# Kernel optimization log

Measured on AMD Instinct MI355X. Metric: run time of the kernel, lower is better.

## Reference

```python
import jax, jax.numpy as jnp
import numpy as np

N_NODES = 50000
N_EDGES = 800000
NEG_SLOPE = 0.2  # PyG GATv2Conv default
EPS = 1e-16      # PyG softmax denominator epsilon


def _segment_softmax(logits, seg, num_segments):
    # logits: [E, H]; seg: [E] target-node ids
    m = jax.ops.segment_max(logits, seg, num_segments=num_segments)
    p = jnp.exp(logits - m[seg])
    s = jax.ops.segment_sum(p, seg, num_segments=num_segments)
    return p / (s[seg] + EPS)


def _gatv2_conv(x, src, dst, Wl, Wr, att, bias, heads, out_ch, concat):
    # x: [N, F]; Wl/Wr: [F, heads*out_ch]; att: [heads, out_ch]
    n = x.shape[0]
    xl = (x @ Wl).reshape(n, heads, out_ch)
    xr = (x @ Wr).reshape(n, heads, out_ch)
    # GATv2: e_ij = att . leaky_relu(xl[j] + xr[i]) for edge j->i
    e = jax.nn.leaky_relu(xl[src] + xr[dst], NEG_SLOPE)  # [E, H, C]
    logit = jnp.einsum('ehc,hc->eh', e, att)             # [E, H]
    alpha = _segment_softmax(logit, dst, n)              # [E, H]
    out = jax.ops.segment_sum(alpha[:, :, None] * xl[src], dst, num_segments=n)  # [N, H, C]
    if concat:
        out = out.reshape(n, heads * out_ch)
    else:
        out = out.mean(axis=1)
    return out + bias


def setup_inputs() -> dict:
    key = jax.random.key(0)
    ks = jax.random.split(key, 20)
    in_ch, hid, out_ch, heads, edge_dim = 128, 128, 64, 8, 6
    c1 = hid // heads  # 16
    g = lambda k, shp, fan: (jax.random.normal(k, shp, jnp.float32) / np.sqrt(fan)).astype(jnp.float32)
    inp = {
        'x': jax.random.normal(ks[0], (N_NODES, in_ch), jnp.float32),
        'edge_index': jax.random.randint(ks[1], (2, N_EDGES), 0, N_NODES, dtype=jnp.int64),
        'edge_attr': jax.random.normal(ks[2], (N_EDGES, edge_dim), jnp.float32),
        'Wl1': g(ks[3], (in_ch, heads * c1), in_ch),
        'Wr1': g(ks[4], (in_ch, heads * c1), in_ch),
        'att1': g(ks[5], (heads, c1), c1),
        'b1': jnp.zeros((heads * c1,), jnp.float32),
        # layer 2: GATv2Conv(hid -> out_ch, heads=1, no concat)
        'Wl2': g(ks[6], (hid, out_ch), hid),
        'Wr2': g(ks[7], (hid, out_ch), hid),
        'att2': g(ks[8], (1, out_ch), out_ch),
        'b2': jnp.zeros((out_ch,), jnp.float32),
        # edge encoder (computed but unused downstream, as in the source)
        'We1': g(ks[9], (edge_dim, hid), edge_dim), 'be1': jnp.zeros((hid,), jnp.float32),
        'We2': g(ks[10], (hid, hid), hid), 'be2': jnp.zeros((hid,), jnp.float32),
        # classifier
        'Wc1': g(ks[11], (out_ch, hid), out_ch), 'bc1': jnp.zeros((hid,), jnp.float32),
        'Wc2': g(ks[12], (hid, 2), hid), 'bc2': jnp.zeros((2,), jnp.float32),
    }
    return inp


def reference(x, edge_index, edge_attr, Wl1, Wr1, att1, b1, Wl2, Wr2, att2, b2,
              We1, be1, We2, be2, Wc1, bc1, Wc2, bc2):
    n = x.shape[0]
    # edge encoder (dead code in the original forward; kept for fidelity)
    _edge_feats = jax.nn.relu(edge_attr @ We1 + be1) @ We2 + be2
    # add self-loops (PyG GATv2Conv default add_self_loops=True)
    loop = jnp.arange(n, dtype=edge_index.dtype)
    src = jnp.concatenate([edge_index[0], loop])
    dst = jnp.concatenate([edge_index[1], loop])
    # layer 1 (heads=8, concat) + relu; dropout is identity in eval
    h = _gatv2_conv(x, src, dst, Wl1, Wr1, att1, b1, heads=8, out_ch=16, concat=True)
    h = jax.nn.relu(h)
    # layer 2 (heads=1, mean)
    emb = _gatv2_conv(h, src, dst, Wl2, Wr2, att2, b2, heads=1, out_ch=64, concat=False)
    logits = jax.nn.relu(emb @ Wc1 + bc1) @ Wc2 + bc2
    return emb, logits
```

## Files before the change

kernel.cpp:

```cpp
#include <hip/hip_runtime.h>
#include <hip/hip_bf16.h>
#include <cfloat>

#define N_NODES 50000
#define N_EDGES 800000
#define E_TOT   850000
#define NEG_SLOPE 0.2f
#define SM_EPS 1e-16f
#define SCAN_B 196

typedef __attribute__((ext_vector_type(8))) short short8;
typedef __attribute__((ext_vector_type(4))) float f32x4;

__device__ __forceinline__ float lrelu(float v) { return v > 0.0f ? v : NEG_SLOPE * v; }

__device__ __forceinline__ unsigned f2bf_pack2(float a, float b) {
    unsigned ua = __float_as_uint(a);
    ua += 0x7fff + ((ua >> 16) & 1);
    unsigned ub = __float_as_uint(b);
    ub += 0x7fff + ((ub >> 16) & 1);
    return (ua >> 16) | (ub & 0xffff0000u);
}
__device__ __forceinline__ unsigned short f2bf(float a) {
    unsigned ua = __float_as_uint(a);
    ua += 0x7fff + ((ua >> 16) & 1);
    return (unsigned short)(ua >> 16);
}
__device__ __forceinline__ float bf_lo(unsigned u) { return __uint_as_float(u << 16); }
__device__ __forceinline__ float bf_hi(unsigned u) { return __uint_as_float(u & 0xffff0000u); }

__device__ __forceinline__ unsigned short pack_one(const float* __restrict__ B0,
                                                   const float* __restrict__ B1,
                                                   int i, int N) {
    int m   = i / (128 * N);
    int rem = i % (128 * N);
    int j    = rem & 7;
    int quad = (rem >> 3) & 3;
    int n    = (rem >> 5) & 15;
    int ctk  = rem >> 9;
    int ct   = ctk % (N / 16);
    int kt   = ctk / (N / 16);
    int k    = kt * 32 + quad * 8 + j;
    int col  = ct * 16 + n;
    const float* B = m ? B1 : B0;
    return f2bf(B[k * N + col]);
}

__global__ void prep(const float* __restrict__ Wl1, const float* __restrict__ Wr1,
                     const float* __restrict__ Wl2, const float* __restrict__ Wr2,
                     unsigned short* __restrict__ Bp1, unsigned short* __restrict__ Bp2,
                     int* __restrict__ deg, int* __restrict__ flags) {
    int i = blockIdx.x * 256 + threadIdx.x;
    if (i < 32768) {
        Bp1[i] = pack_one(Wl1, Wr1, i, 128);
    } else if (i < 49152) {
        Bp2[i - 32768] = pack_one(Wl2, Wr2, i - 32768, 64);
    } else if (i < 99152) {
        deg[i - 49152] = 0;
    } else if (i < 99408) {
        flags[i - 99152] = 0;
    }
}

__device__ __forceinline__ void gemm128_half(int b, const float* __restrict__ x,
                                             const unsigned short* __restrict__ Bm,
                                             unsigned short* __restrict__ Cbf,
                                             float* __restrict__ Cf, int M) {
    int w = threadIdx.x >> 6, lane = threadIdx.x & 63;
    int quad = lane >> 4, l16 = lane & 15;
    int row0 = b * 32 + (w & 1) * 16;
    int cb   = (w >> 1) * 64;
    f32x4 acc[4];
    #pragma unroll
    for (int t = 0; t < 4; ++t) acc[t] = (f32x4){0.f, 0.f, 0.f, 0.f};
    int arow = row0 + l16;
    bool aok = arow < M;
    #pragma unroll
    for (int kt = 0; kt < 4; ++kt) {
        short8 a = (short8)0;
        if (aok) {
            const float* Ap = x + (size_t)arow * 128 + quad * 8 + kt * 32;
            float4 f0 = *(const float4*)(Ap);
            float4 f1 = *(const float4*)(Ap + 4);
            union { uint4 u; short8 s; } cv;
            cv.u.x = f2bf_pack2(f0.x, f0.y);
            cv.u.y = f2bf_pack2(f0.z, f0.w);
            cv.u.z = f2bf_pack2(f1.x, f1.y);
            cv.u.w = f2bf_pack2(f1.z, f1.w);
            a = cv.s;
        }
        #pragma unroll
        for (int t = 0; t < 4; ++t) {
            int ct = (cb >> 4) + t;
            const short* bp = (const short*)Bm + (((kt * 8 + ct) * 16 + l16) * 4 + quad) * 8;
            short8 bfr = *(const short8*)bp;
            acc[t] = __builtin_amdgcn_mfma_f32_16x16x32_bf16(a, bfr, acc[t], 0, 0, 0);
        }
    }
    #pragma unroll
    for (int t = 0; t < 4; ++t) {
        int col = cb + t * 16 + l16;
        #pragma unroll
        for (int r = 0; r < 4; ++r) {
            int row = row0 + quad * 4 + r;
            if (row < M) {
                if (Cbf) Cbf[(size_t)row * 128 + col] = f2bf(acc[t][r]);
                else     Cf[(size_t)row * 128 + col]  = acc[t][r];
            }
        }
    }
}

__global__ __launch_bounds__(256)
void k_count_gemmxl(const int* __restrict__ ei, int* __restrict__ deg,
                    unsigned short* __restrict__ rank16,
                    const float* __restrict__ x, const unsigned short* __restrict__ Bp1,
                    unsigned short* __restrict__ xlbf, int M) {
    int sub = blockIdx.x >> 1;
    if (blockIdx.x & 1) {
        int nz = __syncthreads_or(ei[2 * threadIdx.x + 1]);
        int i = sub * 256 + threadIdx.x;
        if (2 * i >= N_EDGES) return;
        bool has2 = (2 * i + 1 < N_EDGES);
        int d0, d1 = 0;
        if (nz) {
            int2 dp = *(const int2*)(ei + N_EDGES + 2 * i);
            d0 = dp.x; d1 = dp.y;
        } else {
            int4 dp = *(const int4*)(ei + 2 * N_EDGES + 4 * i);
            d0 = dp.x; d1 = dp.z;
        }
        unsigned short r0 = (unsigned short)atomicAdd(&deg[d0], 1);
        unsigned short r1 = 0;
        if (has2) r1 = (unsigned short)atomicAdd(&deg[d1], 1);
        *(unsigned int*)(rank16 + 2 * i) = (unsigned int)r0 | ((unsigned int)r1 << 16);
    } else {
        gemm128_half(sub, x, Bp1, xlbf, nullptr, M);
    }
}

__global__ void scan_fused(const int* __restrict__ deg, int* __restrict__ rowptr,
                           int* __restrict__ esrc, int* __restrict__ bsum,
                           int* __restrict__ flags) {
    __shared__ int sh[256];
    int b = blockIdx.x, t = threadIdx.x, i = b * 256 + t;
    int v = (i < N_NODES) ? deg[i] + 1 : 0;
    sh[t] = v;
    __syncthreads();
    int val = v;
    for (int off = 1; off < 256; off <<= 1) {
        int add = (t >= off) ? sh[t - off] : 0;
        __syncthreads();
        val += add; sh[t] = val;
        __syncthreads();
    }
    if (t == 255) {
        bsum[b] = val;
        __threadfence();
        atomicExch(&flags[b], 1);
    }
    int contrib = 0;
    if (t < b) {
        while (atomicAdd(&flags[t], 0) == 0) {}
        contrib = atomicAdd(&bsum[t], 0);
    }
    __syncthreads();
    sh[t] = contrib;
    __syncthreads();
    #pragma unroll
    for (int off = 128; off; off >>= 1) {
        if (t < off) sh[t] += sh[t + off];
        __syncthreads();
    }
    int offset = sh[0];
    if (i < N_NODES) {
        int rp = (val - v) + offset;
        rowptr[i] = rp;
        esrc[rp] = i;
    }
    if (i == 0) rowptr[N_NODES] = E_TOT;
}

__global__ __launch_bounds__(256)
void k_scatter_gemmxr(const int* __restrict__ ei, const int* __restrict__ rowptr,
                      const unsigned short* __restrict__ rank16, int* __restrict__ esrc,
                      const float* __restrict__ x, const unsigned short* __restrict__ Bp1,
                      float* __restrict__ xr1, int M) {
    int sub = blockIdx.x >> 1;
    if (blockIdx.x & 1) {
        int nz = __syncthreads_or(ei[2 * threadIdx.x + 1]);
        int i = sub * 256 + threadIdx.x;
        if (2 * i >= N_EDGES) return;
        bool has2 = (2 * i + 1 < N_EDGES);
        int s0, d0, s1 = 0, d1 = 0;
        if (nz) {
            int2 sp = *(const int2*)(ei + 2 * i);
            int2 dp = *(const int2*)(ei + N_EDGES + 2 * i);
            s0 = sp.x; s1 = sp.y; d0 = dp.x; d1 = dp.y;
        } else {
            int4 sp = *(const int4*)(ei + 4 * i);
            int4 dp = *(const int4*)(ei + 2 * N_EDGES + 4 * i);
            s0 = sp.x; s1 = sp.z; d0 = dp.x; d1 = dp.z;
        }
        unsigned int rr = *(const unsigned int*)(rank16 + 2 * i);
        esrc[rowptr[d0] + 1 + (int)(rr & 0xffffu)] = s0;
        if (has2) esrc[rowptr[d1] + 1 + (int)(rr >> 16)] = s1;
    } else {
        gemm128_half(sub, x, Bp1 + 128 * 128, nullptr, xr1, M);
    }
}

__global__ __launch_bounds__(256)
void gemm_mfma64(const unsigned short* __restrict__ Abf, const unsigned short* __restrict__ Bp,
                 unsigned short* __restrict__ C0bf, float* __restrict__ C1, int M) {
    int w = threadIdx.x >> 6, lane = threadIdx.x & 63;
    int quad = lane >> 4, l16 = lane & 15;
    int matrix = w >> 1;
    int row0 = blockIdx.x * 32 + (w & 1) * 16;
    const unsigned short* Bm = Bp + matrix * 128 * 64;
    f32x4 acc[4];
    #pragma unroll
    for (int t = 0; t < 4; ++t) acc[t] = (f32x4){0.f, 0.f, 0.f, 0.f};
    int arow = row0 + l16;
    bool aok = arow < M;
    const short* Ap = (const short*)Abf + (size_t)arow * 128 + quad * 8;
    #pragma unroll
    for (int kt = 0; kt < 4; ++kt) {
        short8 a = (short8)0;
        if (aok) a = *(const short8*)(Ap + kt * 32);
        #pragma unroll
        for (int t = 0; t < 4; ++t) {
            const short* bp = (const short*)Bm + (((kt * 4 + t) * 16 + l16) * 4 + quad) * 8;
            short8 bfr = *(const short8*)bp;
            acc[t] = __builtin_amdgcn_mfma_f32_16x16x32_bf16(a, bfr, acc[t], 0, 0, 0);
        }
    }
    #pragma unroll
    for (int t = 0; t < 4; ++t) {
        int col = t * 16 + l16;
        #pragma unroll
        for (int r = 0; r < 4; ++r) {
            int row = row0 + quad * 4 + r;
            if (row < M) {
                if (matrix) C1[(size_t)row * 64 + col] = acc[t][r];
                else        C0bf[(size_t)row * 64 + col] = f2bf(acc[t][r]);
            }
        }
    }
}

__global__ __launch_bounds__(256)
void node_fused1(const int* __restrict__ rowptr, const int* __restrict__ esrc,
                 const unsigned short* __restrict__ xlbf, const float* __restrict__ xr,
                 const float* __restrict__ att, const float* __restrict__ b1,
                 unsigned short* __restrict__ hbf) {
    int wave = threadIdx.x >> 6;
    int lane = threadIdx.x & 63;
    int n = blockIdx.x * 4 + wave;
    int slot = lane >> 4;
    int l = lane & 15;
    int beg = rowptr[n], end = rowptr[n + 1];
    const float* xrp = xr + (size_t)n * 128 + 8 * l;
    float4 xra = *(const float4*)(xrp);
    float4 xrb = *(const float4*)(xrp + 4);
    float4 ata = *(const float4*)(att + 8 * l);
    float4 atb = *(const float4*)(att + 8 * l + 4);
    float den = 0.0f;
    float4 aa = {0, 0, 0, 0}, ab = {0, 0, 0, 0};

    auto body = [&](int k) {
        int s = esrc[k];
        uint4 u = *(const uint4*)(xlbf + (size_t)s * 128 + 8 * l);
        float x0 = bf_lo(u.x), x1 = bf_hi(u.x);
        float x2 = bf_lo(u.y), x3 = bf_hi(u.y);
        float x4 = bf_lo(u.z), x5 = bf_hi(u.z);
        float x6 = bf_lo(u.w), x7 = bf_hi(u.w);
        float v = ata.x * lrelu(x0 + xra.x) + ata.y * lrelu(x1 + xra.y)
                + ata.z * lrelu(x2 + xra.z) + ata.w * lrelu(x3 + xra.w)
                + atb.x * lrelu(x4 + xrb.x) + atb.y * lrelu(x5 + xrb.y)
                + atb.z * lrelu(x6 + xrb.z) + atb.w * lrelu(x7 + xrb.w);
        v += __shfl_xor(v, 1);
        float p = __expf(v);
        den += p;
        aa.x += p * x0; aa.y += p * x1; aa.z += p * x2; aa.w += p * x3;
        ab.x += p * x4; ab.y += p * x5; ab.z += p * x6; ab.w += p * x7;
    };
    int k = beg + slot;
    for (; k + 4 < end; k += 8) { body(k); body(k + 4); }
    if (k < end) body(k);

    #pragma unroll
    for (int off = 16; off < 64; off <<= 1) {
        aa.x += __shfl_xor(aa.x, off); aa.y += __shfl_xor(aa.y, off);
        aa.z += __shfl_xor(aa.z, off); aa.w += __shfl_xor(aa.w, off);
        ab.x += __shfl_xor(ab.x, off); ab.y += __shfl_xor(ab.y, off);
        ab.z += __shfl_xor(ab.z, off); ab.w += __shfl_xor(ab.w, off);
        den   += __shfl_xor(den, off);
    }
    if (slot == 0) {
        float inv = 1.0f / (den + SM_EPS);
        float4 b4a = *(const float4*)(b1 + 8 * l);
        float4 b4b = *(const float4*)(b1 + 8 * l + 4);
        float oa0 = fmaxf(aa.x * inv + b4a.x, 0.0f);
        float oa1 = fmaxf(aa.y * inv + b4a.y, 0.0f);
        float oa2 = fmaxf(aa.z * inv + b4a.z, 0.0f);
        float oa3 = fmaxf(aa.w * inv + b4a.w, 0.0f);
        float ob0 = fmaxf(ab.x * inv + b4b.x, 0.0f);
        float ob1 = fmaxf(ab.y * inv + b4b.y, 0.0f);
        float ob2 = fmaxf(ab.z * inv + b4b.z, 0.0f);
        float ob3 = fmaxf(ab.w * inv + b4b.w, 0.0f);
        uint4 pk;
        pk.x = f2bf_pack2(oa0, oa1);
        pk.y = f2bf_pack2(oa2, oa3);
        pk.z = f2bf_pack2(ob0, ob1);
        pk.w = f2bf_pack2(ob2, ob3);
        *(uint4*)(hbf + (size_t)n * 128 + 8 * l) = pk;
    }
}

__global__ __launch_bounds__(256)
void node_fused2(const int* __restrict__ rowptr, const int* __restrict__ esrc,
                 const unsigned short* __restrict__ xlbf, const float* __restrict__ xr,
                 const float* __restrict__ att, const float* __restrict__ b2v,
                 float* __restrict__ out_emb) {
    int wave = threadIdx.x >> 6;
    int lane = threadIdx.x & 63;
    int n = blockIdx.x * 4 + wave;
    int slot = lane >> 3;
    int l = lane & 7;
    int beg = rowptr[n], end = rowptr[n + 1];
    const float* xrp = xr + (size_t)n * 64 + 8 * l;
    float4 xra = *(const float4*)(xrp);
    float4 xrb = *(const float4*)(xrp + 4);
    float4 ata = *(const float4*)(att + 8 * l);
    float4 atb = *(const float4*)(att + 8 * l + 4);
    float den = 0.0f;
    float4 aa = {0, 0, 0, 0}, ab = {0, 0, 0, 0};

    auto body = [&](int k) {
        int s = esrc[k];
        uint4 u = *(const uint4*)(xlbf + (size_t)s * 64 + 8 * l);
        float x0 = bf_lo(u.x), x1 = bf_hi(u.x);
        float x2 = bf_lo(u.y), x3 = bf_hi(u.y);
        float x4 = bf_lo(u.z), x5 = bf_hi(u.z);
        float x6 = bf_lo(u.w), x7 = bf_hi(u.w);
        float v = ata.x * lrelu(x0 + xra.x) + ata.y * lrelu(x1 + xra.y)
                + ata.z * lrelu(x2 + xra.z) + ata.w * lrelu(x3 + xra.w)
                + atb.x * lrelu(x4 + xrb.x) + atb.y * lrelu(x5 + xrb.y)
                + atb.z * lrelu(x6 + xrb.z) + atb.w * lrelu(x7 + xrb.w);
        v += __shfl_xor(v, 1);
        v += __shfl_xor(v, 2);
        v += __shfl_xor(v, 4);
        float p = __expf(v);
        den += p;
        aa.x += p * x0; aa.y += p * x1; aa.z += p * x2; aa.w += p * x3;
        ab.x += p * x4; ab.y += p * x5; ab.z += p * x6; ab.w += p * x7;
    };
    int k = beg + slot;
    for (; k + 8 < end; k += 16) { body(k); body(k + 8); }
    if (k < end) body(k);

    #pragma unroll
    for (int off = 8; off < 64; off <<= 1) {
        aa.x += __shfl_xor(aa.x, off); aa.y += __shfl_xor(aa.y, off);
        aa.z += __shfl_xor(aa.z, off); aa.w += __shfl_xor(aa.w, off);
        ab.x += __shfl_xor(ab.x, off); ab.y += __shfl_xor(ab.y, off);
        ab.z += __shfl_xor(ab.z, off); ab.w += __shfl_xor(ab.w, off);
        den   += __shfl_xor(den, off);
    }
    if (slot == 0) {
        float inv = 1.0f / (den + SM_EPS);
        float4 b4a = *(const float4*)(b2v + 8 * l);
        float4 b4b = *(const float4*)(b2v + 8 * l + 4);
        float4 ea, eb;
        ea.x = aa.x * inv + b4a.x; ea.y = aa.y * inv + b4a.y;
        ea.z = aa.z * inv + b4a.z; ea.w = aa.w * inv + b4a.w;
        eb.x = ab.x * inv + b4b.x; eb.y = ab.y * inv + b4b.y;
        eb.z = ab.z * inv + b4b.z; eb.w = ab.w * inv + b4b.w;
        float* op = out_emb + (size_t)n * 64 + 8 * l;
        *(float4*)(op)     = ea;
        *(float4*)(op + 4) = eb;
    }
}

#define CLS_NODES 32
__global__ __launch_bounds__(256)
void classifier(const float* __restrict__ emb, const float* __restrict__ Wc1,
                const float* __restrict__ bc1, const float* __restrict__ Wc2,
                const float* __restrict__ bc2, float* __restrict__ out_logits) {
    __shared__ float w1[64 * 128];
    __shared__ float eS[CLS_NODES][64];
    __shared__ float tS[CLS_NODES][132];
    int t = threadIdx.x;
    int n0 = blockIdx.x * CLS_NODES;
    for (int i = t; i < 64 * 128 / 4; i += 256)
        ((float4*)w1)[i] = ((const float4*)Wc1)[i];
    for (int i = t; i < CLS_NODES * 64 / 4; i += 256) {
        size_t off = (size_t)n0 * 64 + i * 4;
        float4 v = {0, 0, 0, 0};
        if (off + 3 < (size_t)N_NODES * 64) v = *(const float4*)(emb + off);
        ((float4*)eS)[i] = v;
    }
    __syncthreads();
    int jj = t & 127, half = t >> 7;
    for (int nn = half; nn < CLS_NODES; nn += 2) {
        float a0 = 0, a1 = 0, a2 = 0, a3 = 0;
        #pragma unroll
        for (int k = 0; k < 64; k += 4) {
            a0 += eS[nn][k]     * w1[(k)     * 128 + jj];
            a1 += eS[nn][k + 1] * w1[(k + 1) * 128 + jj];
            a2 += eS[nn][k + 2] * w1[(k + 2) * 128 + jj];
            a3 += eS[nn][k + 3] * w1[(k + 3) * 128 + jj];
        }
        tS[nn][jj] = fmaxf(bc1[jj] + (a0 + a1) + (a2 + a3), 0.0f);
    }
    __syncthreads();
    int node = t >> 3, seg = t & 7;
    float v0 = 0, v1 = 0;
    #pragma unroll
    for (int c = 0; c < 16; ++c) {
        float tv = tS[node][seg * 16 + c];
        v0 += tv * Wc2[2 * (seg * 16 + c)];
        v1 += tv * Wc2[2 * (seg * 16 + c) + 1];
    }
    v0 += __shfl_xor(v0, 1); v1 += __shfl_xor(v1, 1);
    v0 += __shfl_xor(v0, 2); v1 += __shfl_xor(v1, 2);
    v0 += __shfl_xor(v0, 4); v1 += __shfl_xor(v1, 4);
    int n = n0 + node;
    if (seg == 0 && n < N_NODES) {
        out_logits[(size_t)n * 2 + 0] = v0 + bc2[0];
        out_logits[(size_t)n * 2 + 1] = v1 + bc2[1];
    }
}

extern "C" void kernel_launch(void* const* d_in, const int* in_sizes, int n_in,
                              void* d_out, int out_size, void* d_ws, size_t ws_size,
                              hipStream_t stream) {
    const float* x    = (const float*)d_in[0];
    const int*   ei   = (const int*)d_in[1];
    const float* Wl1  = (const float*)d_in[3];
    const float* Wr1  = (const float*)d_in[4];
    const float* att1 = (const float*)d_in[5];
    const float* b1   = (const float*)d_in[6];
    const float* Wl2  = (const float*)d_in[7];
    const float* Wr2  = (const float*)d_in[8];
    const float* att2 = (const float*)d_in[9];
    const float* b2   = (const float*)d_in[10];
    const float* Wc1  = (const float*)d_in[15];
    const float* bc1  = (const float*)d_in[16];
    const float* Wc2  = (const float*)d_in[17];
    const float* bc2  = (const float*)d_in[18];

    float* ws = (float*)d_ws;
    int* deg    = (int*)ws;
    int* rowptr = deg + 50000;
    int* esrc   = rowptr + 50016;
    int* bsum   = esrc + 850000;
    int* flags  = bsum + 256;
    unsigned short* rank16 = (unsigned short*)(flags + 256);
    float* xr1          = ws + 1400448;
    unsigned short* xlbf = (unsigned short*)(ws + 7800448);
    unsigned short* hbf  = (unsigned short*)(ws + 11000448);
    unsigned short* Bp1  = (unsigned short*)(ws + 14200448);
    unsigned short* Bp2  = (unsigned short*)(ws + 14216832);

    float* out_emb    = (float*)d_out;
    float* out_logits = out_emb + (size_t)N_NODES * 64;

    prep<<<389, 256, 0, stream>>>(Wl1, Wr1, Wl2, Wr2, Bp1, Bp2, deg, flags);

    k_count_gemmxl<<<3126, 256, 0, stream>>>(ei, deg, rank16, x, Bp1, xlbf, N_NODES);

    scan_fused<<<SCAN_B, 256, 0, stream>>>(deg, rowptr, esrc, bsum, flags);

    k_scatter_gemmxr<<<3126, 256, 0, stream>>>(ei, rowptr, rank16, esrc, x, Bp1, xr1, N_NODES);

    node_fused1<<<12500, 256, 0, stream>>>(rowptr, esrc, xlbf, xr1, att1, b1, hbf);

    gemm_mfma64<<<1563, 256, 0, stream>>>(hbf, Bp2, xlbf, xr1, N_NODES);
    node_fused2<<<12500, 256, 0, stream>>>(rowptr, esrc, xlbf, xr1, att2, b2, out_emb);

    classifier<<<1563, 256, 0, stream>>>(out_emb, Wc1, bc1, Wc2, bc2, out_logits);
}
```

Measured before the change: 326.0 us.

## Move classifier to bf16 MFMA, regroup xr GEMM with count pass, use exp2

The classifier's first layer becomes a bf16 MFMA GEMM. It reads a new bf16 copy of the embedding written by node_fused2 and a Wc1 repacked in prep, and folds the ReLU and the second layer into shuffle reductions. The old version staged a 32KB fp32 Wc1 in LDS per block and ran scalar FMAs. The xr GEMM now runs in the degree-count kernel, so the scatter kernel is edge-only. The softmax exponentials use exp2f with att prescaled by log2e. The bf16 classifier input adds rounding error, and the emb output gains an extra write.

```diff
diff --git a/kernel.cpp b/kernel.cpp
--- a/kernel.cpp
+++ b/kernel.cpp
@@ -8,6 +8,7 @@
 #define NEG_SLOPE 0.2f
 #define SM_EPS 1e-16f
 #define SCAN_B 196
+#define LOG2E 1.4426950408889634f
 
 typedef __attribute__((ext_vector_type(8))) short short8;
 typedef __attribute__((ext_vector_type(4))) float f32x4;
@@ -48,17 +49,28 @@
 
 __global__ void prep(const float* __restrict__ Wl1, const float* __restrict__ Wr1,
                      const float* __restrict__ Wl2, const float* __restrict__ Wr2,
+                     const float* __restrict__ Wc1,
                      unsigned short* __restrict__ Bp1, unsigned short* __restrict__ Bp2,
+                     unsigned short* __restrict__ Wc1p,
                      int* __restrict__ deg, int* __restrict__ flags) {
     int i = blockIdx.x * 256 + threadIdx.x;
     if (i < 32768) {
         Bp1[i] = pack_one(Wl1, Wr1, i, 128);
     } else if (i < 49152) {
         Bp2[i - 32768] = pack_one(Wl2, Wr2, i - 32768, 64);
-    } else if (i < 99152) {
-        deg[i - 49152] = 0;
-    } else if (i < 99408) {
-        flags[i - 99152] = 0;
+    } else if (i < 57344) {
+        int idx = i - 49152;
+        int j    = idx & 7;
+        int quad = (idx >> 3) & 3;
+        int n    = (idx >> 5) & 15;
+        int ctk  = idx >> 9;
+        int ct   = ctk & 7;
+        int kt   = ctk >> 3;
+        Wc1p[idx] = f2bf(Wc1[(kt * 32 + quad * 8 + j) * 128 + ct * 16 + n]);
+    } else if (i < 107344) {
+        deg[i - 57344] = 0;
+    } else if (i < 107600) {
+        flags[i - 107344] = 0;
     }
 }
 
@@ -112,12 +124,13 @@
 }
 
 __global__ __launch_bounds__(256)
-void k_count_gemmxl(const int* __restrict__ ei, int* __restrict__ deg,
+void k2_count_gemms(const int* __restrict__ ei, int* __restrict__ deg,
                     unsigned short* __restrict__ rank16,
                     const float* __restrict__ x, const unsigned short* __restrict__ Bp1,
-                    unsigned short* __restrict__ xlbf, int M) {
-    int sub = blockIdx.x >> 1;
-    if (blockIdx.x & 1) {
+                    unsigned short* __restrict__ xlbf, float* __restrict__ xr1, int M) {
+    int kind = blockIdx.x % 3;
+    int sub  = blockIdx.x / 3;
+    if (kind == 1) {
         int nz = __syncthreads_or(ei[2 * threadIdx.x + 1]);
         int i = sub * 256 + threadIdx.x;
         if (2 * i >= N_EDGES) return;
@@ -134,8 +147,10 @@
         unsigned short r1 = 0;
         if (has2) r1 = (unsigned short)atomicAdd(&deg[d1], 1);
         *(unsigned int*)(rank16 + 2 * i) = (unsigned int)r0 | ((unsigned int)r1 << 16);
+    } else if (kind == 0) {
+        gemm128_half(sub, x, Bp1, xlbf, nullptr, M);
     } else {
-        gemm128_half(sub, x, Bp1, xlbf, nullptr, M);
+        gemm128_half(sub, x, Bp1 + 128 * 128, nullptr, xr1, M);
     }
 }
 
@@ -181,33 +196,26 @@
     if (i == 0) rowptr[N_NODES] = E_TOT;
 }
 
-__global__ __launch_bounds__(256)
-void k_scatter_gemmxr(const int* __restrict__ ei, const int* __restrict__ rowptr,
-                      const unsigned short* __restrict__ rank16, int* __restrict__ esrc,
-                      const float* __restrict__ x, const unsigned short* __restrict__ Bp1,
-                      float* __restrict__ xr1, int M) {
-    int sub = blockIdx.x >> 1;
-    if (blockIdx.x & 1) {
-        int nz = __syncthreads_or(ei[2 * threadIdx.x + 1]);
-        int i = sub * 256 + threadIdx.x;
-        if (2 * i >= N_EDGES) return;
-        bool has2 = (2 * i + 1 < N_EDGES);
-        int s0, d0, s1 = 0, d1 = 0;
-        if (nz) {
-            int2 sp = *(const int2*)(ei + 2 * i);
-            int2 dp = *(const int2*)(ei + N_EDGES + 2 * i);
-            s0 = sp.x; s1 = sp.y; d0 = dp.x; d1 = dp.y;
-        } else {
-            int4 sp = *(const int4*)(ei + 4 * i);
-            int4 dp = *(const int4*)(ei + 2 * N_EDGES + 4 * i);
-            s0 = sp.x; s1 = sp.z; d0 = dp.x; d1 = dp.z;
-        }
-        unsigned int rr = *(const unsigned int*)(rank16 + 2 * i);
-        esrc[rowptr[d0] + 1 + (int)(rr & 0xffffu)] = s0;
-        if (has2) esrc[rowptr[d1] + 1 + (int)(rr >> 16)] = s1;
+__global__ void scatter_edges(const int* __restrict__ ei, const int* __restrict__ rowptr,
+                              const unsigned short* __restrict__ rank16,
+                              int* __restrict__ esrc) {
+    int nz = __syncthreads_or(ei[2 * threadIdx.x + 1]);
+    int i = blockIdx.x * blockDim.x + threadIdx.x;
+    if (2 * i >= N_EDGES) return;
+    bool has2 = (2 * i + 1 < N_EDGES);
+    int s0, d0, s1 = 0, d1 = 0;
+    if (nz) {
+        int2 sp = *(const int2*)(ei + 2 * i);
+        int2 dp = *(const int2*)(ei + N_EDGES + 2 * i);
+        s0 = sp.x; s1 = sp.y; d0 = dp.x; d1 = dp.y;
     } else {
-        gemm128_half(sub, x, Bp1 + 128 * 128, nullptr, xr1, M);
-    }
+        int4 sp = *(const int4*)(ei + 4 * i);
+        int4 dp = *(const int4*)(ei + 2 * N_EDGES + 4 * i);
+        s0 = sp.x; s1 = sp.z; d0 = dp.x; d1 = dp.z;
+    }
+    unsigned int rr = *(const unsigned int*)(rank16 + 2 * i);
+    esrc[rowptr[d0] + 1 + (int)(rr & 0xffffu)] = s0;
+    if (has2) esrc[rowptr[d1] + 1 + (int)(rr >> 16)] = s1;
 }
 
 __global__ __launch_bounds__(256)
@@ -265,6 +273,8 @@
     float4 xrb = *(const float4*)(xrp + 4);
     float4 ata = *(const float4*)(att + 8 * l);
     float4 atb = *(const float4*)(att + 8 * l + 4);
+    ata.x *= LOG2E; ata.y *= LOG2E; ata.z *= LOG2E; ata.w *= LOG2E;
+    atb.x *= LOG2E; atb.y *= LOG2E; atb.z *= LOG2E; atb.w *= LOG2E;
     float den = 0.0f;
     float4 aa = {0, 0, 0, 0}, ab = {0, 0, 0, 0};
 
@@ -280,7 +290,7 @@
                 + atb.x * lrelu(x4 + xrb.x) + atb.y * lrelu(x5 + xrb.y)
                 + atb.z * lrelu(x6 + xrb.z) + atb.w * lrelu(x7 + xrb.w);
         v += __shfl_xor(v, 1);
-        float p = __expf(v);
+        float p = exp2f(v);
         den += p;
         aa.x += p * x0; aa.y += p * x1; aa.z += p * x2; aa.w += p * x3;
         ab.x += p * x4; ab.y += p * x5; ab.z += p * x6; ab.w += p * x7;
@@ -322,7 +332,7 @@
 void node_fused2(const int* __restrict__ rowptr, const int* __restrict__ esrc,
                  const unsigned short* __restrict__ xlbf, const float* __restrict__ xr,
                  const float* __restrict__ att, const float* __restrict__ b2v,
-                 float* __restrict__ out_emb) {
+                 float* __restrict__ out_emb, unsigned short* __restrict__ embbf) {
     int wave = threadIdx.x >> 6;
     int lane = threadIdx.x & 63;
     int n = blockIdx.x * 4 + wave;
@@ -334,6 +344,8 @@
     float4 xrb = *(const float4*)(xrp + 4);
     float4 ata = *(const float4*)(att + 8 * l);
     float4 atb = *(const float4*)(att + 8 * l + 4);
+    ata.x *= LOG2E; ata.y *= LOG2E; ata.z *= LOG2E; ata.w *= LOG2E;
+    atb.x *= LOG2E; atb.y *= LOG2E; atb.z *= LOG2E; atb.w *= LOG2E;
     float den = 0.0f;
     float4 aa = {0, 0, 0, 0}, ab = {0, 0, 0, 0};
 
@@ -351,7 +363,7 @@
         v += __shfl_xor(v, 1);
         v += __shfl_xor(v, 2);
         v += __shfl_xor(v, 4);
-        float p = __expf(v);
+        float p = exp2f(v);
         den += p;
         aa.x += p * x0; aa.y += p * x1; aa.z += p * x2; aa.w += p * x3;
         ab.x += p * x4; ab.y += p * x5; ab.z += p * x6; ab.w += p * x7;
@@ -380,56 +392,79 @@
         float* op = out_emb + (size_t)n * 64 + 8 * l;
         *(float4*)(op)     = ea;
         *(float4*)(op + 4) = eb;
-    }
-}
-
-#define CLS_NODES 32
+        uint4 pk;
+        pk.x = f2bf_pack2(ea.x, ea.y);
+        pk.y = f2bf_pack2(ea.z, ea.w);
+        pk.z = f2bf_pack2(eb.x, eb.y);
+        pk.w = f2bf_pack2(eb.z, eb.w);
+        *(uint4*)(embbf + (size_t)n * 64 + 8 * l) = pk;
+    }
+}
+
 __global__ __launch_bounds__(256)
-void classifier(const float* __restrict__ emb, const float* __restrict__ Wc1,
-                const float* __restrict__ bc1, const float* __restrict__ Wc2,
-                const float* __restrict__ bc2, float* __restrict__ out_logits) {
-    __shared__ float w1[64 * 128];
-    __shared__ float eS[CLS_NODES][64];
-    __shared__ float tS[CLS_NODES][132];
+void cls_mfma(const unsigned short* __restrict__ embbf, const unsigned short* __restrict__ Wc1p,
+              const float* __restrict__ bc1, const float* __restrict__ Wc2,
+              const float* __restrict__ bc2, float* __restrict__ out_logits) {
+    __shared__ float part[2][16][2][2];
+    int w = threadIdx.x >> 6, lane = threadIdx.x & 63;
+    int quad = lane >> 4, l16 = lane & 15;
+    int rowhalf = w & 1, colhalf = w >> 1;
+    int row0 = blockIdx.x * 32 + rowhalf * 16;
+    int cb = colhalf * 64;
+    f32x4 acc[4];
+    #pragma unroll
+    for (int t = 0; t < 4; ++t) acc[t] = (f32x4){0.f, 0.f, 0.f, 0.f};
+    int arow = row0 + l16;
+    bool aok = arow < N_NODES;
+    const short* Ap = (const short*)embbf + (size_t)arow * 64 + quad * 8;
+    #pragma unroll
+    for (int kt = 0; kt < 2; ++kt) {
+        short8 a = (short8)0;
+        if (aok) a = *(const short8*)(Ap + kt * 32);
+        #pragma unroll
+        for (int t = 0; t < 4; ++t) {
+            int ct = colhalf * 4 + t;
+            const short* bp = (const short*)Wc1p + (((kt * 8 + ct) * 16 + l16) * 4 + quad) * 8;
+            short8 bfr = *(const short8*)bp;
+            acc[t] = __builtin_amdgcn_mfma_f32_16x16x32_bf16(a, bfr, acc[t], 0, 0, 0);
+        }
+    }
+    float p0[4] = {0, 0, 0, 0}, p1[4] = {0, 0, 0, 0};
+    #pragma unroll
+    for (int t = 0; t < 4; ++t) {
+        int col = cb + t * 16 + l16;
+        float w2a = Wc2[2 * col], w2b = Wc2[2 * col + 1];
+        float bc = bc1[col];
+        #pragma unroll
+        for (int r = 0; r < 4; ++r) {
+            float tv = fmaxf(acc[t][r] + bc, 0.0f);
+            p0[r] += tv * w2a;
+            p1[r] += tv * w2b;
+        }
+    }
+    #pragma unroll
+    for (int off = 1; off < 16; off <<= 1) {
+        #pragma unroll
+        for (int r = 0; r < 4; ++r) {
+            p0[r] += __shfl_xor(p0[r], off);
+            p1[r] += __shfl_xor(p1[r], off);
+        }
+    }
+    if (l16 == 0) {
+        #pragma unroll
+        for (int r = 0; r < 4; ++r) {
+            part[rowhalf][quad * 4 + r][colhalf][0] = p0[r];
+            part[rowhalf][quad * 4 + r][colhalf][1] = p1[r];
+        }
+    }
+    __syncthreads();
     int t = threadIdx.x;
-    int n0 = blockIdx.x * CLS_NODES;
-    for (int i = t; i < 64 * 128 / 4; i += 256)
-        ((float4*)w1)[i] = ((const float4*)Wc1)[i];
-    for (int i = t; i < CLS_NODES * 64 / 4; i += 256) {
-        size_t off = (size_t)n0 * 64 + i * 4;
-        float4 v = {0, 0, 0, 0};
-        if (off + 3 < (size_t)N_NODES * 64) v = *(const float4*)(emb + off);
-        ((float4*)eS)[i] = v;
-    }
-    __syncthreads();
-    int jj = t & 127, half = t >> 7;
-    for (int nn = half; nn < CLS_NODES; nn += 2) {
-        float a0 = 0, a1 = 0, a2 = 0, a3 = 0;
-        #pragma unroll
-        for (int k = 0; k < 64; k += 4) {
-            a0 += eS[nn][k]     * w1[(k)     * 128 + jj];
-            a1 += eS[nn][k + 1] * w1[(k + 1) * 128 + jj];
-            a2 += eS[nn][k + 2] * w1[(k + 2) * 128 + jj];
-            a3 += eS[nn][k + 3] * w1[(k + 3) * 128 + jj];
-        }
-        tS[nn][jj] = fmaxf(bc1[jj] + (a0 + a1) + (a2 + a3), 0.0f);
-    }
-    __syncthreads();
-    int node = t >> 3, seg = t & 7;
-    float v0 = 0, v1 = 0;
-    #pragma unroll
-    for (int c = 0; c < 16; ++c) {
-        float tv = tS[node][seg * 16 + c];
-        v0 += tv * Wc2[2 * (seg * 16 + c)];
-        v1 += tv * Wc2[2 * (seg * 16 + c) + 1];
-    }
-    v0 += __shfl_xor(v0, 1); v1 += __shfl_xor(v1, 1);
-    v0 += __shfl_xor(v0, 2); v1 += __shfl_xor(v1, 2);
-    v0 += __shfl_xor(v0, 4); v1 += __shfl_xor(v1, 4);
-    int n = n0 + node;
-    if (seg == 0 && n < N_NODES) {
-        out_logits[(size_t)n * 2 + 0] = v0 + bc2[0];
-        out_logits[(size_t)n * 2 + 1] = v1 + bc2[1];
+    if (t < 64) {
+        int row = t >> 1, c = t & 1;
+        int rh = row >> 4, r16 = row & 15;
+        float s = part[rh][r16][0][c] + part[rh][r16][1][c] + bc2[c];
+        int n = blockIdx.x * 32 + row;
+        if (n < N_NODES) out_logits[(size_t)n * 2 + c] = s;
     }
 }
 
@@ -458,27 +493,29 @@
     int* bsum   = esrc + 850000;
     int* flags  = bsum + 256;
     unsigned short* rank16 = (unsigned short*)(flags + 256);
-    float* xr1          = ws + 1400448;
+    float* xr1           = ws + 1400448;
     unsigned short* xlbf = (unsigned short*)(ws + 7800448);
     unsigned short* hbf  = (unsigned short*)(ws + 11000448);
-    unsigned short* Bp1  = (unsigned short*)(ws + 14200448);
-    unsigned short* Bp2  = (unsigned short*)(ws + 14216832);
+    unsigned short* Bp1   = (unsigned short*)(ws + 14200448);
+    unsigned short* Bp2   = (unsigned short*)(ws + 14216832);
+    unsigned short* Wc1p  = (unsigned short*)(ws + 14225024);
+    unsigned short* embbf = (unsigned short*)(ws + 14229120);
 
     float* out_emb    = (float*)d_out;
     float* out_logits = out_emb + (size_t)N_NODES * 64;
 
-    prep<<<389, 256, 0, stream>>>(Wl1, Wr1, Wl2, Wr2, Bp1, Bp2, deg, flags);
-
-    k_count_gemmxl<<<3126, 256, 0, stream>>>(ei, deg, rank16, x, Bp1, xlbf, N_NODES);
+    prep<<<421, 256, 0, stream>>>(Wl1, Wr1, Wl2, Wr2, Wc1, Bp1, Bp2, Wc1p, deg, flags);
+
+    k2_count_gemms<<<4689, 256, 0, stream>>>(ei, deg, rank16, x, Bp1, xlbf, xr1, N_NODES);
 
     scan_fused<<<SCAN_B, 256, 0, stream>>>(deg, rowptr, esrc, bsum, flags);
 
-    k_scatter_gemmxr<<<3126, 256, 0, stream>>>(ei, rowptr, rank16, esrc, x, Bp1, xr1, N_NODES);
+    scatter_edges<<<1563, 256, 0, stream>>>(ei, rowptr, rank16, esrc);
 
     node_fused1<<<12500, 256, 0, stream>>>(rowptr, esrc, xlbf, xr1, att1, b1, hbf);
 
     gemm_mfma64<<<1563, 256, 0, stream>>>(hbf, Bp2, xlbf, xr1, N_NODES);
-    node_fused2<<<12500, 256, 0, stream>>>(rowptr, esrc, xlbf, xr1, att2, b2, out_emb);
-
-    classifier<<<1563, 256, 0, stream>>>(out_emb, Wc1, bc1, Wc2, bc2, out_logits);
-}
+    node_fused2<<<12500, 256, 0, stream>>>(rowptr, esrc, xlbf, xr1, att2, b2, out_emb, embbf);
+
+    cls_mfma<<<1563, 256, 0, stream>>>(embbf, Wc1p, bc1, Wc2, bc2, out_logits);
+}
```

New measurement: 300.3 us. 7.9% less time.
